# Kernel optimization log

Hardware: AMD Instinct MI355X
Metric: run time of the kernel (lower is better)

The kernel has to match this reference:

```python
import jax, jax.numpy as jnp
import numpy as np

N_NODES = 200_000
N_EDGES = 400_000
EXTRA_NNZ = 3 * N_EDGES
IN_CH = 14
HID = 128
ALPHA = -1.5  # HNHN edge-cardinality exponent
BETA = -0.5   # HNHN node-cardinality exponent


def setup_inputs() -> dict:
    key = jax.random.key(0)
    ks = jax.random.split(key, 16)
    # COO incidence: guarantee every node and every edge has >= 1 entry so
    # cardinality^negative_power stays finite (like real molecular hypergraphs).
    base_rows = jnp.arange(N_NODES, dtype=jnp.int32)
    base_cols = jnp.arange(N_NODES, dtype=jnp.int32) % N_EDGES
    edge_rows = jax.random.randint(ks[0], (N_EDGES,), 0, N_NODES, dtype=jnp.int32)
    edge_cols = jnp.arange(N_EDGES, dtype=jnp.int32)
    rnd_rows = jax.random.randint(ks[1], (EXTRA_NNZ,), 0, N_NODES, dtype=jnp.int32)
    rnd_cols = jax.random.randint(ks[2], (EXTRA_NNZ,), 0, N_EDGES, dtype=jnp.int32)
    inc_rows = jnp.concatenate([base_rows, edge_rows, rnd_rows])
    inc_cols = jnp.concatenate([base_cols, edge_cols, rnd_cols])
    inc_vals = jnp.ones(inc_rows.shape[0], dtype=jnp.float32)

    def glorot(k, shape):
        fan_in, fan_out = shape[0], shape[-1]
        s = jnp.sqrt(2.0 / (fan_in + fan_out)).astype(jnp.float32)
        return jax.random.normal(k, shape, dtype=jnp.float32) * s

    return {
        "x_0": jax.random.normal(ks[3], (N_NODES, IN_CH), dtype=jnp.float32),
        "inc_rows": inc_rows,
        "inc_cols": inc_cols,
        "inc_vals": inc_vals,
        "w0_l1": glorot(ks[4], (IN_CH, HID)),
        "w1_l1": glorot(ks[5], (HID, HID)),
        "b1_l1": glorot(ks[6], (1, HID)),
        "b0_l1": glorot(ks[7], (1, HID)),
        "w0_l2": glorot(ks[8], (HID, HID)),
        "w1_l2": glorot(ks[9], (HID, HID)),
        "b1_l2": glorot(ks[10], (1, HID)),
        "b0_l2": glorot(ks[11], (1, HID)),
        "lin_w": glorot(ks[12], (HID, 1)),
        "lin_b": jnp.zeros((1,), dtype=jnp.float32),
    }


def _normalized_values(inc_rows, inc_cols, inc_vals):
    """HNHN alpha/beta normalization of B (node<-edge) and B^T (edge<-node)."""
    seg = jax.ops.segment_sum
    deg_e = seg(inc_vals, inc_cols, num_segments=N_EDGES)   # |e| per hyperedge
    deg_v = seg(inc_vals, inc_rows, num_segments=N_NODES)   # |v| per node
    e_card = deg_e ** ALPHA
    n_card = deg_v ** BETA
    denom_v = seg(inc_vals * e_card[inc_cols], inc_rows, num_segments=N_NODES)  # (B @ e_card)
    denom_e = seg(inc_vals * n_card[inc_rows], inc_cols, num_segments=N_EDGES)  # (B^T @ n_card)
    # D0_left_alpha^{-1} B D1_right_alpha   and   D1_left_beta^{-1} B^T D0_right_beta
    vals_v_from_e = inc_vals * e_card[inc_cols] / denom_v[inc_rows]
    vals_e_from_v = inc_vals * n_card[inc_rows] / denom_e[inc_cols]
    return vals_v_from_e, vals_e_from_v


def reference(x_0, inc_rows, inc_cols, inc_vals,
              w0_l1, w1_l1, b1_l1, b0_l1,
              w0_l2, w1_l2, b1_l2, b0_l2,
              lin_w, lin_b):
    seg = jax.ops.segment_sum
    vals_v_from_e, vals_e_from_v = _normalized_values(inc_rows, inc_cols, inc_vals)

    def layer(x0, w0, w1, b1, b0):
        # node -> hyperedge: x1 = sigma(Bt_norm @ (x0 W0) + b1)
        m = x0 @ w0                                        # [N_NODES, HID]
        x1 = jax.nn.sigmoid(
            seg(vals_e_from_v[:, None] * m[inc_rows], inc_cols, num_segments=N_EDGES) + b1
        )                                                  # [N_EDGES, HID]
        # hyperedge -> node: x0' = sigma(B_norm @ (x1 W1) + b0)
        m2 = x1 @ w1
        x0n = jax.nn.sigmoid(
            seg(vals_v_from_e[:, None] * m2[inc_cols], inc_rows, num_segments=N_NODES) + b0
        )                                                  # [N_NODES, HID]
        return x0n, x1

    x0, x1 = layer(x_0, w0_l1, w1_l1, b1_l1, b0_l1)
    x0, x1 = layer(x0, w0_l2, w1_l2, b1_l2, b0_l2)
    pooled = jnp.max(x0, axis=0)                           # graph-level max pool [HID]
    return pooled @ lin_w + lin_b                          # [1]
```

## Files before the change

### kernel.cpp

```cpp
#include <hip/hip_runtime.h>
#include <hip/hip_bf16.h>

#define N_NODES 200000
#define N_EDGES 400000
#define HID 128

#define SHIFT 10
#define NB_E 391
#define NB_V 196
#define NBT (NB_E + NB_V)
#define CAP_E 6144
#define CAP_V 10240

typedef unsigned int u32;
typedef unsigned short u16;
typedef unsigned char u8;
typedef long long i64;
typedef __attribute__((ext_vector_type(4))) float f32x4;
typedef __attribute__((ext_vector_type(2))) float f32x2;

__device__ inline float sigmoidf(float v) { return 1.0f / (1.0f + __expf(-v)); }

__device__ inline u32 pk4_fp8(float f0, float f1, float f2, float f3) {
  u32 v = __builtin_amdgcn_cvt_pk_fp8_f32(f0, f1, 0, false);
  v = __builtin_amdgcn_cvt_pk_fp8_f32(f2, f3, v, true);
  return v;
}

__device__ inline void acc16_fp8(const uint4& q, float wv, float* a) {
#pragma unroll
  for (int h = 0; h < 4; ++h) {
    u32 u = (&q.x)[h];
    f32x2 p0 = __builtin_amdgcn_cvt_pk_f32_fp8(u, false);
    f32x2 p1 = __builtin_amdgcn_cvt_pk_f32_fp8(u, true);
    a[h * 4 + 0] = fmaf(wv, p0.x, a[h * 4 + 0]);
    a[h * 4 + 1] = fmaf(wv, p0.y, a[h * 4 + 1]);
    a[h * 4 + 2] = fmaf(wv, p1.x, a[h * 4 + 2]);
    a[h * 4 + 3] = fmaf(wv, p1.y, a[h * 4 + 3]);
  }
}

__global__ __launch_bounds__(256) void bin_kernel(
    const int* __restrict__ rows, const int* __restrict__ cols,
    const float* __restrict__ vals, u32* __restrict__ bkE,
    u32* __restrict__ bkV, int2* __restrict__ tmp_e, int2* __restrict__ tmp_v,
    int nnz) {
  __shared__ u32 h[NBT];
  __shared__ u32 base[NBT];
  const int tid = threadIdx.x;
  for (int j = tid; j < NBT; j += 256) h[j] = 0;
  __syncthreads();
  const int i0 = blockIdx.x * 4096;
  for (int k = 0; k < 16; ++k) {
    int i = i0 + k * 256 + tid;
    if (i < nnz) {
      atomicAdd(&h[cols[i] >> SHIFT], 1u);
      atomicAdd(&h[NB_E + (rows[i] >> SHIFT)], 1u);
    }
  }
  __syncthreads();
  for (int j = tid; j < NBT; j += 256) {
    u32 n = h[j];
    base[j] = n ? ((j < NB_E) ? atomicAdd(&bkE[j], n)
                              : atomicAdd(&bkV[j - NB_E], n))
                : 0;
    h[j] = 0;
  }
  __syncthreads();
  for (int k = 0; k < 16; ++k) {
    int i = i0 + k * 256 + tid;
    if (i < nnz) {
      int c = cols[i], r = rows[i];
      int vb = __float_as_int(vals[i]);
      int be = c >> SHIFT;
      int bv = NB_E + (r >> SHIFT);
      u32 le = atomicAdd(&h[be], 1u);
      tmp_e[(size_t)be * CAP_E + base[be] + le] =
          make_int2(((c & 1023) << 19) | r, vb);
      u32 lv = atomicAdd(&h[bv], 1u);
      tmp_v[(size_t)(bv - NB_E) * CAP_V + base[bv] + lv] =
          make_int2(((r & 1023) << 19) | c, vb);
    }
  }
}

__global__ __launch_bounds__(512) void scan_small_kernel(u32* __restrict__ blk, int n) {
  __shared__ u32 tmp[512];
  int t = threadIdx.x;
  u32 v = (t < n) ? blk[t] : 0;
  tmp[t] = v;
  __syncthreads();
  for (int d = 1; d < 512; d <<= 1) {
    u32 x = (t >= d) ? tmp[t - d] : 0;
    __syncthreads();
    tmp[t] += x;
    __syncthreads();
  }
  if (t < n) blk[t] = tmp[t] - v;
}

__global__ void set4_kernel(u32* __restrict__ bkE, u32* __restrict__ bkV,
                            u32* __restrict__ ptr_e, u32* __restrict__ ptr_v,
                            u32 nnz) {
  bkE[NB_E] = nnz;
  bkV[NB_V] = nnz;
  ptr_e[N_EDGES] = nnz;
  ptr_v[N_NODES] = nnz;
}

template <bool EDGE>
__global__ __launch_bounds__(512) void build_kernel(
    const int2* __restrict__ tmp, int cap, const u32* __restrict__ bukBase,
    u32* __restrict__ ptr, int2* __restrict__ ent, float* __restrict__ card,
    const float* __restrict__ ncard, int S) {
  __shared__ u32 loc[1024];
  __shared__ u32 sstart[1024];
  __shared__ u32 aux[512];
  const int tid = threadIdx.x;
  const int c0 = blockIdx.x << SHIFT;
  const int nseg = min(1024, S - c0);
  const u32 eb = bukBase[blockIdx.x], ee = bukBase[blockIdx.x + 1];
  const u32 cnt = ee - eb;
  const int2* tp = tmp + (size_t)blockIdx.x * cap;
  loc[tid] = 0;
  loc[tid + 512] = 0;
  __syncthreads();
  for (u32 j = tid; j < cnt; j += 512)
    atomicAdd(&loc[(u32)tp[j].x >> 19], 1u);
  __syncthreads();
  u32 a0 = loc[2 * tid], a1 = loc[2 * tid + 1];
  u32 T = a0 + a1;
  aux[tid] = T;
  __syncthreads();
  for (int d = 1; d < 512; d <<= 1) {
    u32 x = (tid >= d) ? aux[tid - d] : 0;
    __syncthreads();
    aux[tid] += x;
    __syncthreads();
  }
  u32 off = aux[tid] - T;
  loc[2 * tid] = off;
  loc[2 * tid + 1] = off + a0;
  sstart[2 * tid] = off;
  sstart[2 * tid + 1] = off + a0;
  __syncthreads();
  for (int k = tid; k < nseg; k += 512) ptr[c0 + k] = eb + loc[k];
  __syncthreads();
  for (u32 j = tid; j < cnt; j += 512) {
    int2 e = tp[j];
    u32 s = (u32)e.x >> 19;
    u32 p = atomicAdd(&loc[s], 1u);
    ent[eb + p] = make_int2(e.x & 0x7FFFF, e.y);
  }
  __syncthreads();
  for (int k = tid; k < nseg; k += 512) {
    u32 s0 = eb + sstart[k], s1 = eb + loc[k];
    float s = 0.f;
    for (u32 j = s0; j < s1; ++j) s += __int_as_float(ent[j].y);
    float t = rsqrtf(s);
    card[c0 + k] = EDGE ? t * t * t : t;
    if (EDGE) {
      float d = 0.f;
      for (u32 j = s0; j < s1; ++j) {
        int2 en = ent[j];
        d += __int_as_float(en.y) * ncard[en.x];
      }
      float inv = 1.f / d;
      for (u32 j = s0; j < s1; ++j) {
        int2 en = ent[j];
        ent[j].y = __float_as_int(__int_as_float(en.y) * ncard[en.x] * inv);
      }
    }
  }
}

__global__ __launch_bounds__(256) void segV_kernel(
    const u32* __restrict__ ptr_v, int2* __restrict__ ent_v,
    const float* __restrict__ e_card) {
  int t = blockIdx.x * 256 + threadIdx.x;
  int i = t >> 1;
  int half = t & 1;
  if (i >= N_NODES) return;
  u32 b = ptr_v[i], e = ptr_v[i + 1];
  float s = 0.f;
  for (u32 j = b + half; j < e; j += 2) {
    int2 en = ent_v[j];
    s += __int_as_float(en.y) * e_card[en.x];
  }
  s += __shfl_xor(s, 1);
  float inv = 1.f / s;
  for (u32 j = b + half; j < e; j += 2) {
    int2 en = ent_v[j];
    ent_v[j].y = __float_as_int(__int_as_float(en.y) * e_card[en.x] * inv);
  }
}


__global__ __launch_bounds__(256) void mm14n_kernel(
    const float* __restrict__ x0, const float* __restrict__ w,
    u8* __restrict__ U, int N) {
  __shared__ float ws[14 * HID];
  const int tid = threadIdx.x;
  for (int i = tid; i < 14 * HID; i += 256) ws[i] = w[i];
  __syncthreads();
  const int row = blockIdx.x * 8 + (tid >> 5);
  const int c4 = (tid & 31) << 2;
  if (row >= N) return;
  const float* xr = x0 + (size_t)row * 14;
  float a0 = 0.f, a1 = 0.f, a2 = 0.f, a3 = 0.f;
#pragma unroll
  for (int k = 0; k < 14; ++k) {
    const float xv = xr[k];
    const float* wr = ws + k * HID + c4;
    a0 = fmaf(xv, wr[0], a0);
    a1 = fmaf(xv, wr[1], a1);
    a2 = fmaf(xv, wr[2], a2);
    a3 = fmaf(xv, wr[3], a3);
  }
  *(u32*)(U + (size_t)row * HID + c4) = pk4_fp8(a0, a1, a2, a3);
}

__device__ inline void load_wfrags(const float* __restrict__ w, int lo, int hi,
                                   i64 wf[8][4]) {
#pragma unroll
  for (int n = 0; n < 8; ++n)
#pragma unroll
    for (int t = 0; t < 4; ++t) {
      const float* wp = w + (size_t)(t * 32 + hi * 8) * HID + n * 16 + lo;
      u32 w0 = pk4_fp8(wp[0], wp[HID], wp[2 * HID], wp[3 * HID]);
      u32 w1 = pk4_fp8(wp[4 * HID], wp[5 * HID], wp[6 * HID], wp[7 * HID]);
      wf[n][t] = (i64)w0 | ((i64)w1 << 32);
    }
}

template <bool SIG, bool POOL>
__global__ __launch_bounds__(256, 1) void im128_mfma_kernel(
    u8* __restrict__ buf, const float* __restrict__ w,
    const float* __restrict__ b, u32* __restrict__ pooled, int R) {
  const int tid = threadIdx.x;
  const int wave = tid >> 6;
  const int lo = tid & 15;
  const int hi = (tid & 63) >> 4;
  i64 wf[8][4];
  load_wfrags(w, lo, hi, wf);
  float bias[8];
  if (SIG) {
#pragma unroll
    for (int n = 0; n < 8; ++n) bias[n] = b[n * 16 + lo];
  }
  float pm[8];
#pragma unroll
  for (int n = 0; n < 8; ++n) pm[n] = 0.f;

  for (int rb = blockIdx.x * 64 + wave * 16; rb < R; rb += gridDim.x * 64) {
    const u8* xp = buf + (size_t)(rb + lo) * HID + hi * 8;
    i64 a0 = *(const i64*)(xp);
    i64 a1 = *(const i64*)(xp + 32);
    i64 a2 = *(const i64*)(xp + 64);
    i64 a3 = *(const i64*)(xp + 96);
    u8* yp = buf + (size_t)(rb + hi * 4) * HID + lo;
#pragma unroll
    for (int n = 0; n < 8; ++n) {
      f32x4 c = {0.f, 0.f, 0.f, 0.f};
      c = __builtin_amdgcn_mfma_f32_16x16x32_fp8_fp8(a0, wf[n][0], c, 0, 0, 0);
      c = __builtin_amdgcn_mfma_f32_16x16x32_fp8_fp8(a1, wf[n][1], c, 0, 0, 0);
      c = __builtin_amdgcn_mfma_f32_16x16x32_fp8_fp8(a2, wf[n][2], c, 0, 0, 0);
      c = __builtin_amdgcn_mfma_f32_16x16x32_fp8_fp8(a3, wf[n][3], c, 0, 0, 0);
#pragma unroll
      for (int r = 0; r < 4; ++r) {
        float v = SIG ? sigmoidf(c[r] + bias[n]) : c[r];
        if (POOL) {
          pm[n] = fmaxf(pm[n], v);
        } else {
          u32 q = __builtin_amdgcn_cvt_pk_fp8_f32(v, v, 0, false);
          yp[(size_t)r * HID + n * 16] = (u8)q;
        }
      }
    }
  }

  if (POOL) {
    __shared__ u32 pmax[HID];
    for (int i = tid; i < HID; i += 256) pmax[i] = 0;
    __syncthreads();
#pragma unroll
    for (int n = 0; n < 8; ++n)
      atomicMax(&pmax[n * 16 + lo], __float_as_uint(pm[n]));
    __syncthreads();
    if (tid < HID) atomicMax(&pooled[tid], pmax[tid]);
  }
}


template <bool SIG>
__global__ __launch_bounds__(256) void gather128_kernel(
    const u32* __restrict__ ptr, const int2* __restrict__ ent,
    const u8* __restrict__ src, const float* __restrict__ b,
    u8* __restrict__ dst, int S) {
  long long t = (long long)blockIdx.x * 256 + threadIdx.x;
  int r = (int)(t >> 3);
  if (r >= S) return;
  const int c16 = (int)(t & 7) << 4;
  u32 beg = ptr[r], end = ptr[r + 1];
  float a[16];
#pragma unroll
  for (int i = 0; i < 16; ++i) a[i] = 0.f;
  u32 j = beg;
  for (; j + 2 <= end; j += 2) {
    int2 e0 = ent[j];
    int2 e1 = ent[j + 1];
    const uint4 q0 = *(const uint4*)(src + (size_t)e0.x * HID + c16);
    const uint4 q1 = *(const uint4*)(src + (size_t)e1.x * HID + c16);
    acc16_fp8(q0, __int_as_float(e0.y), a);
    acc16_fp8(q1, __int_as_float(e1.y), a);
  }
  if (j < end) {
    int2 e0 = ent[j];
    const uint4 q0 = *(const uint4*)(src + (size_t)e0.x * HID + c16);
    acc16_fp8(q0, __int_as_float(e0.y), a);
  }
  if (SIG) {
#pragma unroll
    for (int h = 0; h < 4; ++h) {
      float4 bb = *(const float4*)(b + c16 + h * 4);
      a[h * 4 + 0] = sigmoidf(a[h * 4 + 0] + bb.x);
      a[h * 4 + 1] = sigmoidf(a[h * 4 + 1] + bb.y);
      a[h * 4 + 2] = sigmoidf(a[h * 4 + 2] + bb.z);
      a[h * 4 + 3] = sigmoidf(a[h * 4 + 3] + bb.w);
    }
  }
  uint4 pk;
  pk.x = pk4_fp8(a[0], a[1], a[2], a[3]);
  pk.y = pk4_fp8(a[4], a[5], a[6], a[7]);
  pk.z = pk4_fp8(a[8], a[9], a[10], a[11]);
  pk.w = pk4_fp8(a[12], a[13], a[14], a[15]);
  *(uint4*)(dst + (size_t)r * HID + c16) = pk;
}


__global__ __launch_bounds__(128) void final_kernel(
    const u32* __restrict__ pooled, const float* __restrict__ lin_w,
    const float* __restrict__ lin_b, float* __restrict__ out) {
  __shared__ float red[64];
  int t = threadIdx.x;
  float v = __uint_as_float(pooled[t]) * lin_w[t];
  if (t >= 64) red[t - 64] = v;
  __syncthreads();
  if (t < 64) {
    v += red[t];
#pragma unroll
    for (int off = 32; off > 0; off >>= 1) v += __shfl_down(v, off);
    if (t == 0) out[0] = v + lin_b[0];
  }
}

__global__ void diag_kernel(float* out, float v) { out[0] = v; }


extern "C" void kernel_launch(void* const* d_in, const int* in_sizes, int n_in,
                              void* d_out, int out_size, void* d_ws, size_t ws_size,
                              hipStream_t stream) {
  const float* x0     = (const float*)d_in[0];
  const int*   rows   = (const int*)d_in[1];
  const int*   cols   = (const int*)d_in[2];
  const float* vals   = (const float*)d_in[3];
  const float* w0_l1  = (const float*)d_in[4];
  const float* w1_l1  = (const float*)d_in[5];
  const float* b1_l1  = (const float*)d_in[6];
  const float* b0_l1  = (const float*)d_in[7];
  const float* w0_l2  = (const float*)d_in[8];
  const float* w1_l2  = (const float*)d_in[9];
  const float* b1_l2  = (const float*)d_in[10];
  const float* b0_l2  = (const float*)d_in[11];
  const float* lin_w  = (const float*)d_in[12];
  const float* lin_b  = (const float*)d_in[13];
  float* out = (float*)d_out;
  const int nnz = in_sizes[1];

  char* wsp = (char*)d_ws;
  size_t off = 0;
  auto carve = [&](size_t bytes) -> char* {
    char* p = wsp + off;
    off = (off + bytes + 511) & ~(size_t)511;
    return p;
  };
  float* n_card  = (float*)carve((size_t)N_NODES * 4);
  float* e_card  = (float*)carve((size_t)N_EDGES * 4);
  u32*   ptr_v   = (u32*)carve((size_t)(N_NODES + 1) * 4);
  u32*   ptr_e   = (u32*)carve((size_t)(N_EDGES + 1) * 4);
  u32*   bkE     = (u32*)carve((NB_E + 1) * 4);
  u32*   bkV     = (u32*)carve((NB_V + 1) * 4);
  int2*  ent_v   = (int2*)carve((size_t)nnz * 8);
  int2*  ent_e   = (int2*)carve((size_t)nnz * 8);
  u32*   pooled  = (u32*)carve(HID * 4);
  u8*    bufN    = (u8*)carve((size_t)N_NODES * HID);
  u8*    bufE    = (u8*)carve((size_t)N_EDGES * HID);
  int2*  tmp_e   = (int2*)carve((size_t)NB_E * CAP_E * 8);
  int2*  tmp_v   = (int2*)carve((size_t)NB_V * CAP_V * 8);

  if (off > ws_size) {
    diag_kernel<<<1, 1, 0, stream>>>(out, (float)(ws_size >> 20));
    return;
  }

  hipMemsetAsync(bkE, 0, (NB_E + 1) * 4, stream);
  hipMemsetAsync(bkV, 0, (NB_V + 1) * 4, stream);
  hipMemsetAsync(pooled, 0, HID * 4, stream);

  const int nbBin = (nnz + 4095) / 4096;

  bin_kernel<<<nbBin, 256, 0, stream>>>(rows, cols, vals, bkE, bkV,
                                        tmp_e, tmp_v, nnz);
  scan_small_kernel<<<1, 512, 0, stream>>>(bkE, NB_E);
  scan_small_kernel<<<1, 512, 0, stream>>>(bkV, NB_V);
  set4_kernel<<<1, 1, 0, stream>>>(bkE, bkV, ptr_e, ptr_v, (u32)nnz);
  build_kernel<false><<<NB_V, 512, 0, stream>>>(tmp_v, CAP_V, bkV, ptr_v,
                                                ent_v, n_card, nullptr, N_NODES);
  build_kernel<true><<<NB_E, 512, 0, stream>>>(tmp_e, CAP_E, bkE, ptr_e,
                                               ent_e, e_card, n_card, N_EDGES);
  segV_kernel<<<(2 * N_NODES + 255) / 256, 256, 0, stream>>>(ptr_v, ent_v, e_card);

  const int nbE8 = (int)(((long long)N_EDGES * 8 + 255) / 256);
  const int nbN8 = (int)(((long long)N_NODES * 8 + 255) / 256);

  mm14n_kernel<<<N_NODES / 8, 256, 0, stream>>>(x0, w0_l1, bufN, N_NODES);
  gather128_kernel<true><<<nbE8, 256, 0, stream>>>(ptr_e, ent_e, bufN,
                                                   b1_l1, bufE, N_EDGES);
  gather128_kernel<false><<<nbN8, 256, 0, stream>>>(ptr_v, ent_v, bufE,
                                                    nullptr, bufN, N_NODES);
  im128_mfma_kernel<true, false><<<1024, 256, 0, stream>>>(bufN, w1_l1, b0_l1,
                                                           nullptr, N_NODES);

  im128_mfma_kernel<false, false><<<1024, 256, 0, stream>>>(bufN, w0_l2, nullptr,
                                                            nullptr, N_NODES);
  gather128_kernel<true><<<nbE8, 256, 0, stream>>>(ptr_e, ent_e, bufN,
                                                   b1_l2, bufE, N_EDGES);
  gather128_kernel<false><<<nbN8, 256, 0, stream>>>(ptr_v, ent_v, bufE,
                                                    nullptr, bufN, N_NODES);
  im128_mfma_kernel<true, true><<<1024, 256, 0, stream>>>(bufN, w1_l2, b0_l2,
                                                          pooled, N_NODES);

  final_kernel<<<1, 128, 0, stream>>>(pooled, lin_w, lin_b, out);
}
```

Baseline: 471.6 us.

## Fuse hyperedge-to-node gather with following 128x128 MFMA matmul

Replaces the separate node-side gather kernel and the subsequent FP8 MFMA matmul with a single gmm_kernel. Each wave gathers and accumulates 16 node rows in registers, packs them to FP8 and feeds them directly into MFMA with sigmoid and bias applied, and pools in the final layer. This removes one write and one read of the 200k x 128 intermediate node buffer per layer, plus a launch. The trade-off is one row per lane with 32 accumulators, serial per-row loops that can load-imbalance across lanes, and launch bounds of one block per SIMD that may reduce occupancy for latency hiding.

```diff
diff --git a/kernel.cpp b/kernel.cpp
--- a/kernel.cpp
+++ b/kernel.cpp
@@ -16,6 +16,7 @@
 typedef unsigned short u16;
 typedef unsigned char u8;
 typedef long long i64;
+typedef unsigned long long u64;
 typedef __attribute__((ext_vector_type(4))) float f32x4;
 typedef __attribute__((ext_vector_type(2))) float f32x2;
 
@@ -38,6 +39,19 @@
     a[h * 4 + 2] = fmaf(wv, p1.x, a[h * 4 + 2]);
     a[h * 4 + 3] = fmaf(wv, p1.y, a[h * 4 + 3]);
   }
+}
+
+__device__ inline void acc8_fp8(i64 q, float wv, float* a) {
+  u32 u0 = (u32)(u64)q;
+  u32 u1 = (u32)((u64)q >> 32);
+  f32x2 p0 = __builtin_amdgcn_cvt_pk_f32_fp8(u0, false);
+  f32x2 p1 = __builtin_amdgcn_cvt_pk_f32_fp8(u0, true);
+  f32x2 p2 = __builtin_amdgcn_cvt_pk_f32_fp8(u1, false);
+  f32x2 p3 = __builtin_amdgcn_cvt_pk_f32_fp8(u1, true);
+  a[0] = fmaf(wv, p0.x, a[0]); a[1] = fmaf(wv, p0.y, a[1]);
+  a[2] = fmaf(wv, p1.x, a[2]); a[3] = fmaf(wv, p1.y, a[3]);
+  a[4] = fmaf(wv, p2.x, a[4]); a[5] = fmaf(wv, p2.y, a[5]);
+  a[6] = fmaf(wv, p3.x, a[6]); a[7] = fmaf(wv, p3.y, a[7]);
 }
 
 __global__ __launch_bounds__(256) void bin_kernel(
@@ -274,6 +288,108 @@
         } else {
           u32 q = __builtin_amdgcn_cvt_pk_fp8_f32(v, v, 0, false);
           yp[(size_t)r * HID + n * 16] = (u8)q;
+        }
+      }
+    }
+  }
+
+  if (POOL) {
+    __shared__ u32 pmax[HID];
+    for (int i = tid; i < HID; i += 256) pmax[i] = 0;
+    __syncthreads();
+#pragma unroll
+    for (int n = 0; n < 8; ++n)
+      atomicMax(&pmax[n * 16 + lo], __float_as_uint(pm[n]));
+    __syncthreads();
+    if (tid < HID) atomicMax(&pooled[tid], pmax[tid]);
+  }
+}
+
+template <bool POOL>
+__global__ __launch_bounds__(256, 1) void gmm_kernel(
+    const u32* __restrict__ ptr, const int2* __restrict__ ent,
+    const u8* __restrict__ src, const float* __restrict__ w,
+    const float* __restrict__ b, u8* __restrict__ dst,
+    u32* __restrict__ pooled, int R) {
+  const int tid = threadIdx.x;
+  const int wave = tid >> 6;
+  const int lo = tid & 15;
+  const int hi = (tid & 63) >> 4;
+  i64 wf[8][4];
+  load_wfrags(w, lo, hi, wf);
+  float bias[8];
+#pragma unroll
+  for (int n = 0; n < 8; ++n) bias[n] = b[n * 16 + lo];
+  float pm[8];
+#pragma unroll
+  for (int n = 0; n < 8; ++n) pm[n] = 0.f;
+
+  for (int rb = blockIdx.x * 64 + wave * 16; rb < R; rb += gridDim.x * 64) {
+    const int r = rb + lo;
+    u32 jb = ptr[r], je = ptr[r + 1];
+    float acc[32];
+#pragma unroll
+    for (int i = 0; i < 32; ++i) acc[i] = 0.f;
+    u32 j = jb;
+    for (; j + 2 <= je; j += 2) {
+      int2 e0 = ent[j];
+      int2 e1 = ent[j + 1];
+      const u8* s0 = src + (size_t)e0.x * HID + hi * 8;
+      const u8* s1 = src + (size_t)e1.x * HID + hi * 8;
+      i64 q00 = *(const i64*)(s0);
+      i64 q01 = *(const i64*)(s0 + 32);
+      i64 q02 = *(const i64*)(s0 + 64);
+      i64 q03 = *(const i64*)(s0 + 96);
+      i64 q10 = *(const i64*)(s1);
+      i64 q11 = *(const i64*)(s1 + 32);
+      i64 q12 = *(const i64*)(s1 + 64);
+      i64 q13 = *(const i64*)(s1 + 96);
+      float w0 = __int_as_float(e0.y), w1 = __int_as_float(e1.y);
+      acc8_fp8(q00, w0, acc +  0);
+      acc8_fp8(q01, w0, acc +  8);
+      acc8_fp8(q02, w0, acc + 16);
+      acc8_fp8(q03, w0, acc + 24);
+      acc8_fp8(q10, w1, acc +  0);
+      acc8_fp8(q11, w1, acc +  8);
+      acc8_fp8(q12, w1, acc + 16);
+      acc8_fp8(q13, w1, acc + 24);
+    }
+    if (j < je) {
+      int2 e0 = ent[j];
+      const u8* s0 = src + (size_t)e0.x * HID + hi * 8;
+      i64 q00 = *(const i64*)(s0);
+      i64 q01 = *(const i64*)(s0 + 32);
+      i64 q02 = *(const i64*)(s0 + 64);
+      i64 q03 = *(const i64*)(s0 + 96);
+      float w0 = __int_as_float(e0.y);
+      acc8_fp8(q00, w0, acc +  0);
+      acc8_fp8(q01, w0, acc +  8);
+      acc8_fp8(q02, w0, acc + 16);
+      acc8_fp8(q03, w0, acc + 24);
+    }
+    i64 A[4];
+#pragma unroll
+    for (int t = 0; t < 4; ++t) {
+      u32 p0 = pk4_fp8(acc[t * 8 + 0], acc[t * 8 + 1], acc[t * 8 + 2], acc[t * 8 + 3]);
+      u32 p1 = pk4_fp8(acc[t * 8 + 4], acc[t * 8 + 5], acc[t * 8 + 6], acc[t * 8 + 7]);
+      A[t] = (i64)p0 | ((i64)p1 << 32);
+    }
+    u8* yp = dst + (size_t)(rb + hi * 4) * HID + lo;
+#pragma unroll
+    for (int n = 0; n < 8; ++n) {
+      f32x4 c = {0.f, 0.f, 0.f, 0.f};
+      c = __builtin_amdgcn_mfma_f32_16x16x32_fp8_fp8(A[0], wf[n][0], c, 0, 0, 0);
+      c = __builtin_amdgcn_mfma_f32_16x16x32_fp8_fp8(A[1], wf[n][1], c, 0, 0, 0);
+      c = __builtin_amdgcn_mfma_f32_16x16x32_fp8_fp8(A[2], wf[n][2], c, 0, 0, 0);
+      c = __builtin_amdgcn_mfma_f32_16x16x32_fp8_fp8(A[3], wf[n][3], c, 0, 0, 0);
+#pragma unroll
+      for (int r4 = 0; r4 < 4; ++r4) {
+        float v = sigmoidf(c[r4] + bias[n]);
+        if (POOL) {
+          pm[n] = fmaxf(pm[n], v);
+        } else {
+          u32 q = __builtin_amdgcn_cvt_pk_fp8_f32(v, v, 0, false);
+          yp[(size_t)r4 * HID + n * 16] = (u8)q;
         }
       }
     }
@@ -421,24 +537,19 @@
   segV_kernel<<<(2 * N_NODES + 255) / 256, 256, 0, stream>>>(ptr_v, ent_v, e_card);
 
   const int nbE8 = (int)(((long long)N_EDGES * 8 + 255) / 256);
-  const int nbN8 = (int)(((long long)N_NODES * 8 + 255) / 256);
 
   mm14n_kernel<<<N_NODES / 8, 256, 0, stream>>>(x0, w0_l1, bufN, N_NODES);
   gather128_kernel<true><<<nbE8, 256, 0, stream>>>(ptr_e, ent_e, bufN,
                                                    b1_l1, bufE, N_EDGES);
-  gather128_kernel<false><<<nbN8, 256, 0, stream>>>(ptr_v, ent_v, bufE,
-                                                    nullptr, bufN, N_NODES);
-  im128_mfma_kernel<true, false><<<1024, 256, 0, stream>>>(bufN, w1_l1, b0_l1,
-                                                           nullptr, N_NODES);
+  gmm_kernel<false><<<1024, 256, 0, stream>>>(ptr_v, ent_v, bufE, w1_l1,
+                                              b0_l1, bufN, nullptr, N_NODES);
 
   im128_mfma_kernel<false, false><<<1024, 256, 0, stream>>>(bufN, w0_l2, nullptr,
                                                             nullptr, N_NODES);
   gather128_kernel<true><<<nbE8, 256, 0, stream>>>(ptr_e, ent_e, bufN,
                                                    b1_l2, bufE, N_EDGES);
-  gather128_kernel<false><<<nbN8, 256, 0, stream>>>(ptr_v, ent_v, bufE,
-                                                    nullptr, bufN, N_NODES);
-  im128_mfma_kernel<true, true><<<1024, 256, 0, stream>>>(bufN, w1_l2, b0_l2,
-                                                          pooled, N_NODES);
+  gmm_kernel<true><<<1024, 256, 0, stream>>>(ptr_v, ent_v, bufE, w1_l2,
+                                             b0_l2, nullptr, pooled, N_NODES);
 
   final_kernel<<<1, 128, 0, stream>>>(pooled, lin_w, lin_b, out);
 }
```

After: 513.7 us. +8.9%, slower.
